# Kernel optimization log

Hardware: AMD Instinct MI355X
Metric: run time of the kernel (lower is better)

Reference implementation:

```python
import jax, jax.numpy as jnp
import numpy as np

EPS = 0.1
C, H, W = 3, 64, 64


def setup_inputs() -> dict:
    key = jax.random.key(0)
    x = jax.random.uniform(key, (C, H, W), dtype=jnp.float32)  # pixels in [0,1)
    return {"x": x}


def reference(x):
    # Faithful translation of TransformedInput.forward.
    N = x.shape[0] * x.shape[1] * x.shape[2]
    lo = jax.nn.relu(EPS - x) * 0.5          # clip-below correction
    hi = jax.nn.relu(x - (1.0 - EPS)) * 0.5  # clip-above correction
    center = x + lo - hi                     # zonotope center (row 0)
    err = EPS - lo - hi                      # per-pixel error magnitude

    cond = (err >= 0).reshape(-1)            # selection mask (flattened, row-major = loop order)
    # Stream compaction: selected element k gets row 1 + (# selected strictly before k).
    # Inclusive cumsum of the mask equals exactly that (starting at 1) for selected entries.
    rows = jnp.where(cond, jnp.cumsum(cond.astype(jnp.int32)), N + 1)  # N+1 is OOB -> dropped

    zono = jnp.zeros((1 + N, N), dtype=x.dtype)
    zono = zono.at[0].set(center.reshape(-1))
    zono = zono.at[rows, jnp.arange(N)].set(err.reshape(-1), mode="drop")
    return zono.reshape(1 + N, x.shape[0], x.shape[1], x.shape[2])
```

## Files before the change

kernel.cpp:

```cpp
#include <hip/hip_runtime.h>

#define EPS_F 0.1f
#define SCAN_THREADS 1024
#define SCAN_ITEMS 12

__global__ __launch_bounds__(SCAN_THREADS) void finalize_kernel(
    const float* __restrict__ x,
    float* __restrict__ out,
    int N)
{
    __shared__ int wave_sums[16];

    const int t    = threadIdx.x;
    const int lane = t & 63;
    const int wave = t >> 6;
    const int base = t * SCAN_ITEMS;

    float c_[SCAN_ITEMS], e_[SCAN_ITEMS];
    int   cnd[SCAN_ITEMS];

    int local = 0;
    #pragma unroll
    for (int i = 0; i < SCAN_ITEMS; i++) {
        float xv = x[base + i];
        float lo = fmaxf(EPS_F - xv, 0.0f) * 0.5f;
        float hi = fmaxf(xv - (1.0f - EPS_F), 0.0f) * 0.5f;
        c_[i] = xv + lo - hi;
        float ev = EPS_F - lo - hi;
        e_[i] = ev;
        cnd[i] = (ev >= 0.0f) ? 1 : 0;
        local += cnd[i];
    }

    int inc = local;
    #pragma unroll
    for (int off = 1; off < 64; off <<= 1) {
        int y = __shfl_up(inc, off, 64);
        if (lane >= off) inc += y;
    }
    if (lane == 63) wave_sums[wave] = inc;
    __syncthreads();

    if (t == 0) {
        int acc = 0;
        #pragma unroll
        for (int w = 0; w < 16; w++) {
            acc += wave_sums[w];
            wave_sums[w] = acc;
        }
    }
    __syncthreads();

    const int wave_off = (wave == 0) ? 0 : wave_sums[wave - 1];
    int run = wave_off + (inc - local);

    #pragma unroll
    for (int i = 0; i < SCAN_ITEMS; i++) {
        const int k = base + i;
        out[k] = c_[i];
        run += cnd[i];
        if (cnd[i]) {
            out[(size_t)run * (size_t)N + (size_t)k] = e_[i];
        }
    }
}

extern "C" void kernel_launch(void* const* d_in, const int* in_sizes, int n_in,
                              void* d_out, int out_size, void* d_ws, size_t ws_size,
                              hipStream_t stream)
{
    const float* x = (const float*)d_in[0];
    float* out = (float*)d_out;
    const int N = in_sizes[0];

    const size_t out_bytes = (size_t)(N + 1) * (size_t)N * sizeof(float);
    hipMemsetAsync(d_out, 0, out_bytes, stream);

    finalize_kernel<<<1, SCAN_THREADS, 0, stream>>>(x, out, N);
}
```

Before: 578.3 us.

## Replace memset plus scatter with row-wise fused zero-and-fill kernel using inverse map

Splits the work into a single-block scan kernel that computes center/error values and an inverse row-to-column map in workspace, followed by a wide grid kernel that writes every output row exactly once with float4 stores, placing the single nonzero inline. This removes the separate full-buffer memset and the serialized scattered writes from a single block. It adds a workspace dependency and a second launch, and keeps the old path as a fallback when workspace is insufficient.

```diff
diff --git a/kernel.cpp b/kernel.cpp
--- a/kernel.cpp
+++ b/kernel.cpp
@@ -3,6 +3,112 @@
 #define EPS_F 0.1f
 #define SCAN_THREADS 1024
 #define SCAN_ITEMS 12
+#define FILL_THREADS 256
+#define FILL_BLOCKS 2048
+
+__global__ __launch_bounds__(SCAN_THREADS) void scan_kernel(
+    const float* __restrict__ x,
+    float* __restrict__ center,
+    float* __restrict__ err,
+    int*   __restrict__ inv,
+    int N)
+{
+    __shared__ int wave_sums[16];
+
+    const int t    = threadIdx.x;
+    const int lane = t & 63;
+    const int wave = t >> 6;
+    const int base = t * SCAN_ITEMS;
+
+    for (int r = t; r <= N; r += SCAN_THREADS) inv[r] = -1;
+
+    float c_[SCAN_ITEMS], e_[SCAN_ITEMS];
+    int   cnd[SCAN_ITEMS];
+
+    int local = 0;
+    #pragma unroll
+    for (int i = 0; i < SCAN_ITEMS; i++) {
+        float xv = x[base + i];
+        float lo = fmaxf(EPS_F - xv, 0.0f) * 0.5f;
+        float hi = fmaxf(xv - (1.0f - EPS_F), 0.0f) * 0.5f;
+        c_[i] = xv + lo - hi;
+        float ev = EPS_F - lo - hi;
+        e_[i] = ev;
+        cnd[i] = (ev >= 0.0f) ? 1 : 0;
+        local += cnd[i];
+    }
+
+    #pragma unroll
+    for (int i = 0; i < SCAN_ITEMS; i++) {
+        center[base + i] = c_[i];
+        err[base + i]    = e_[i];
+    }
+
+    int inc = local;
+    #pragma unroll
+    for (int off = 1; off < 64; off <<= 1) {
+        int y = __shfl_up(inc, off, 64);
+        if (lane >= off) inc += y;
+    }
+    if (lane == 63) wave_sums[wave] = inc;
+    __syncthreads();
+
+    if (t == 0) {
+        int acc = 0;
+        #pragma unroll
+        for (int w = 0; w < 16; w++) {
+            acc += wave_sums[w];
+            wave_sums[w] = acc;
+        }
+    }
+    __syncthreads();
+
+    const int wave_off = (wave == 0) ? 0 : wave_sums[wave - 1];
+    int run = wave_off + (inc - local);
+
+    #pragma unroll
+    for (int i = 0; i < SCAN_ITEMS; i++) {
+        run += cnd[i];
+        if (cnd[i]) inv[run] = base + i;
+    }
+}
+
+__global__ __launch_bounds__(FILL_THREADS) void zono_write(
+    float* __restrict__ out,
+    const float* __restrict__ center,
+    const float* __restrict__ err,
+    const int*   __restrict__ inv,
+    int N)
+{
+    const int nvec = N >> 2;
+
+    for (int row = blockIdx.x; row <= N; row += gridDim.x) {
+        float4* __restrict__ dst =
+            reinterpret_cast<float4*>(out + (size_t)row * (size_t)N);
+
+        if (row == 0) {
+            const float4* __restrict__ c4 =
+                reinterpret_cast<const float4*>(center);
+            for (int v = threadIdx.x; v < nvec; v += FILL_THREADS)
+                dst[v] = c4[v];
+        } else {
+            const int colsel = inv[row];
+            const int v4sel  = colsel >> 2;
+            const float ev   = (colsel >= 0) ? err[colsel] : 0.0f;
+            for (int v = threadIdx.x; v < nvec; v += FILL_THREADS) {
+                float4 z = make_float4(0.0f, 0.0f, 0.0f, 0.0f);
+                if (v == v4sel) {
+                    const int c0 = v4sel << 2;
+                    z.x = (colsel == c0 + 0) ? ev : 0.0f;
+                    z.y = (colsel == c0 + 1) ? ev : 0.0f;
+                    z.z = (colsel == c0 + 2) ? ev : 0.0f;
+                    z.w = (colsel == c0 + 3) ? ev : 0.0f;
+                }
+                dst[v] = z;
+            }
+        }
+    }
+}
 
 __global__ __launch_bounds__(SCAN_THREADS) void finalize_kernel(
     const float* __restrict__ x,
@@ -73,8 +179,20 @@
     float* out = (float*)d_out;
     const int N = in_sizes[0];
 
-    const size_t out_bytes = (size_t)(N + 1) * (size_t)N * sizeof(float);
-    hipMemsetAsync(d_out, 0, out_bytes, stream);
+    const size_t need_ws = (size_t)N * 4 + (size_t)N * 4 + (size_t)(N + 1) * 4;
 
-    finalize_kernel<<<1, SCAN_THREADS, 0, stream>>>(x, out, N);
+    if (d_ws != nullptr && ws_size >= need_ws) {
+        float* center = (float*)d_ws;
+        float* err    = center + N;
+        int*   inv    = (int*)(err + N);
+
+        scan_kernel<<<1, SCAN_THREADS, 0, stream>>>(x, center, err, inv, N);
+
+        zono_write<<<FILL_BLOCKS, FILL_THREADS, 0, stream>>>(
+            out, center, err, inv, N);
+    } else {
+        const size_t out_bytes = (size_t)(N + 1) * (size_t)N * sizeof(float);
+        hipMemsetAsync(d_out, 0, out_bytes, stream);
+        finalize_kernel<<<1, SCAN_THREADS, 0, stream>>>(x, out, N);
+    }
 }
```

After: 594.0 us. 1.03x slower.
